# Optimization experiments

Measured on AMD Instinct MI355X. Metric: run time of the kernel, lower is better.

## Reference

```python
import jax, jax.numpy as jnp
import numpy as np

N_NODES = 50000
N_EDGES = 800000
IN_CH = 256
OUT_CH = 128
HID = 2 * OUT_CH  # 256
N_GRAPHS = 64


def setup_inputs() -> dict:
    key = jax.random.key(0)
    k = jax.random.split(key, 8)
    x = jax.random.normal(k[0], (N_NODES, IN_CH), dtype=jnp.float32)
    edge_index = jax.random.randint(k[1], (2, N_EDGES), 0, N_NODES, dtype=jnp.int64)
    batch = jnp.sort(jax.random.randint(k[2], (N_NODES,), 0, N_GRAPHS, dtype=jnp.int64))
    # GCNConv parameters (glorot-ish init)
    W1 = jax.random.normal(k[3], (IN_CH, HID), dtype=jnp.float32) / np.sqrt(IN_CH)
    b1 = jnp.zeros((HID,), dtype=jnp.float32)
    W2 = jax.random.normal(k[4], (HID, OUT_CH), dtype=jnp.float32) / np.sqrt(HID)
    b2 = jnp.zeros((OUT_CH,), dtype=jnp.float32)
    return {"x": x, "W1": W1, "b1": b1, "W2": W2, "b2": b2,
            "edge_index": edge_index, "batch": batch}


def _gcn_conv(x, W, b, src, dst, n):
    """PyG GCNConv: transform, then sym-normalized aggregation with self-loops."""
    h = x @ W  # [N, F_out]
    # degree over destination nodes, including the added self-loop
    deg = jnp.zeros((n,), dtype=h.dtype).at[dst].add(1.0) + 1.0
    dinv = jax.lax.rsqrt(deg)
    norm = dinv[src] * dinv[dst]            # [E]
    agg = jnp.zeros_like(h).at[dst].add(h[src] * norm[:, None])
    agg = agg + h * (1.0 / deg)[:, None]    # self-loop contribution: deg_i^{-1}
    return agg + b


def reference(x, W1, b1, W2, b2, edge_index, batch):
    src, dst = edge_index[0], edge_index[1]
    # dropout is identity in eval mode (training=False)
    h = jax.nn.elu(_gcn_conv(x, W1, b1, src, dst, N_NODES))
    h = _gcn_conv(h, W2, b2, src, dst, N_NODES)
    # global mean pool over graphs
    ones = jnp.ones((N_NODES,), dtype=h.dtype)
    counts = jax.ops.segment_sum(ones, batch, num_segments=N_GRAPHS)
    sums = jax.ops.segment_sum(h, batch, num_segments=N_GRAPHS)
    return sums / jnp.maximum(counts, 1.0)[:, None]
```

## Files before the change

### kernel.cpp

```cpp
#include <hip/hip_runtime.h>
#include <hip/hip_bf16.h>

#define N_NODES 50000
#define N_EDGES 800000
#define IN_CH 256
#define HID 256
#define OUT_CH 128
#define N_GRAPHS 64
#define SCAN_BLOCKS 196
#define M_PAD 50048
#define COUNT_BLOCKS 3125
#define CVTX_BLOCKS  12512
#define GEMM1_BLOCKS 782
#define SROW 50048
#define S_QUARTER 12512
#define GEMM2_BLOCKS 391
#define SBUILD_BLOCKS 256
#define T2_BLOCKS 391
#define T2_KC 128
#define RED_BLOCKS 128

typedef __bf16 bf16x8 __attribute__((ext_vector_type(8)));
typedef float f32x4 __attribute__((ext_vector_type(4)));
typedef float f32x2 __attribute__((ext_vector_type(2)));
typedef unsigned short u16x8 __attribute__((ext_vector_type(8)));

__device__ __forceinline__ float bf2f(unsigned short u) {
    union { unsigned int i; float f; } x; x.i = ((unsigned int)u) << 16; return x.f;
}
__device__ __forceinline__ unsigned short f2bf(float f) {
    union { float f; unsigned int i; } x; x.f = f;
    unsigned int r = x.i + 0x7FFFu + ((x.i >> 16) & 1u);
    return (unsigned short)(r >> 16);
}

__device__ __forceinline__ float lo_f(unsigned int u) {
    return __uint_as_float(u << 16);
}
__device__ __forceinline__ float hi_f(unsigned int u) {
    return __uint_as_float(u & 0xFFFF0000u);
}

__device__ __forceinline__ void load16(const void* g, void* l) {
    __builtin_amdgcn_global_load_lds(
        (const __attribute__((address_space(1))) void*)g,
        (__attribute__((address_space(3))) void*)l, 16, 0, 0);
}

__device__ __forceinline__ int rp(const int* __restrict__ rl,
                                  const int* __restrict__ boff, int i) {
    return rl[i] + boff[i >> 8];
}

__global__ __launch_bounds__(256) void count_cvtx_kernel(const int* __restrict__ ei,
                                                         int* __restrict__ cnt,
                                                         int* __restrict__ erank,
                                                         const float* __restrict__ x,
                                                         unsigned short* __restrict__ xb) {
    int b = blockIdx.x;
    if (b < COUNT_BLOCKS) {
        int e = b * 256 + threadIdx.x;
        erank[e] = atomicAdd(&cnt[ei[N_EDGES + e]], 1);
        return;
    }
    int i = (b - COUNT_BLOCKS) * 256 + threadIdx.x;
    ushort4 o;
    if (i < N_NODES * (IN_CH / 4)) {
        float4 v = ((const float4*)x)[i];
        o.x = f2bf(v.x); o.y = f2bf(v.y); o.z = f2bf(v.z); o.w = f2bf(v.w);
    } else {
        o = make_ushort4(0, 0, 0, 0);
    }
    ((ushort4*)xb)[i] = o;
}

__global__ __launch_bounds__(256) void scan_a_kernel(const int* __restrict__ cnt,
                                                     int* __restrict__ rl,
                                                     int* __restrict__ blocksum,
                                                     float* __restrict__ dinv,
                                                     float* __restrict__ invdeg,
                                                     const int* __restrict__ batch,
                                                     int* __restrict__ rstart) {
    __shared__ int tmp[256];
    int t = threadIdx.x;
    int i = blockIdx.x * 256 + t;
    int v = (i < N_NODES) ? cnt[i] : 0;
    int x = v;
    tmp[t] = x;
    __syncthreads();
    if (i < N_NODES) {
        int bg = batch[i];
        int bp = (i > 0) ? batch[i - 1] : -1;
        for (int g = bp + 1; g <= bg; g++) rstart[g] = i;
        if (i == N_NODES - 1)
            for (int g = bg + 1; g <= N_GRAPHS; g++) rstart[g] = N_NODES;
    }
#pragma unroll
    for (int off = 1; off < 256; off <<= 1) {
        int y = (t >= off) ? tmp[t - off] : 0;
        __syncthreads();
        x += y;
        tmp[t] = x;
        __syncthreads();
    }
    if (i <= N_NODES) rl[i] = x - v;
    if (i < N_NODES) {
        float d = (float)v + 1.0f;
        dinv[i] = rsqrtf(d);
        invdeg[i] = 1.0f / d;
    }
    if (t == 255) blocksum[blockIdx.x] = x;
}

__global__ __launch_bounds__(256) void scanb_cvtw_kernel(
        const int* __restrict__ blocksum, int* __restrict__ blockoff,
        const float* __restrict__ W1, const float* __restrict__ W2,
        unsigned short* __restrict__ w1t, unsigned short* __restrict__ w2t) {
    int t = threadIdx.x;
    if (blockIdx.x < 384) {
        int i = blockIdx.x * 256 + t;
        if (i < HID * IN_CH) {
            int n = i >> 8, k = i & 255;
            w1t[i] = f2bf(W1[k * HID + n]);
        } else {
            int j = i - HID * IN_CH;
            int n = j >> 8, k = j & 255;
            w2t[j] = f2bf(W2[k * OUT_CH + n]);
        }
        return;
    }
    __shared__ int tmp[256];
    int v = (t < SCAN_BLOCKS) ? blocksum[t] : 0;
    int x = v;
    tmp[t] = x;
    __syncthreads();
#pragma unroll
    for (int off = 1; off < 256; off <<= 1) {
        int y = (t >= off) ? tmp[t - off] : 0;
        __syncthreads();
        x += y;
        tmp[t] = x;
        __syncthreads();
    }
    if (t < SCAN_BLOCKS) blockoff[t] = x - v;
}

template <int TR>
__device__ __forceinline__ void gemm_body(const unsigned short* __restrict__ A,
                                          const unsigned short* __restrict__ Bt,
                                          unsigned short* __restrict__ C,
                                          int N, int bxx, int byy, char* As, char* Bs) {
    const int K = 256;
    int tid = threadIdx.x;
    int bm = bxx * 128;
    int bn = byy * 128;
    int lane = tid & 63, wave = tid >> 6;
    int lane15 = lane & 15, quad = lane >> 4;
    int wm0 = (wave >> 1) << 6;
    int wn0 = (wave & 1) << 6;

    int s1 = tid, s2 = tid + 256;
    int r1 = s1 >> 2, q1 = (s1 & 3) ^ ((r1 >> 1) & 3);
    int r2 = s2 >> 2, q2 = (s2 & 3) ^ ((r2 >> 1) & 3);
    const char* gA1 = (const char*)(A + (size_t)(bm + r1) * K) + (q1 << 4);
    const char* gA2 = (const char*)(A + (size_t)(bm + r2) * K) + (q2 << 4);
    const char* gB1 = (const char*)(Bt + (size_t)(bn + r1) * K) + (q1 << 4);
    const char* gB2 = (const char*)(Bt + (size_t)(bn + r2) * K) + (q2 << 4);
    char* lA1 = As + (wave << 10);
    char* lA2 = As + 4096 + (wave << 10);
    char* lB1 = Bs + (wave << 10);
    char* lB2 = Bs + 4096 + (wave << 10);

    int swm = (lane15 >> 1) & 3;
    f32x4 acc[4][4];
#pragma unroll
    for (int mt = 0; mt < 4; mt++)
#pragma unroll
        for (int nt = 0; nt < 4; nt++)
            acc[mt][nt] = (f32x4){0.f, 0.f, 0.f, 0.f};

    for (int k0 = 0; k0 < K; k0 += 32) {
        __syncthreads();
        load16(gA1 + (k0 << 1), lA1);
        load16(gA2 + (k0 << 1), lA2);
        load16(gB1 + (k0 << 1), lB1);
        load16(gB2 + (k0 << 1), lB2);
        __syncthreads();
        bf16x8 af[4], bfr[4];
#pragma unroll
        for (int t = 0; t < 4; t++) {
            int ra = wm0 + t * 16 + lane15;
            af[t] = *(const bf16x8*)(As + ra * 64 + ((quad ^ swm) << 4));
            int rb = wn0 + t * 16 + lane15;
            bfr[t] = *(const bf16x8*)(Bs + rb * 64 + ((quad ^ swm) << 4));
        }
#pragma unroll
        for (int mt = 0; mt < 4; mt++)
#pragma unroll
            for (int nt = 0; nt < 4; nt++)
                acc[mt][nt] = __builtin_amdgcn_mfma_f32_16x16x32_bf16(
                    af[mt], bfr[nt], acc[mt][nt], 0, 0, 0);
    }

#pragma unroll
    for (int mt = 0; mt < 4; mt++) {
        int rowb = bm + wm0 + mt * 16 + quad * 4;
#pragma unroll
        for (int nt = 0; nt < 4; nt++) {
            int col = bn + wn0 + nt * 16 + lane15;
            f32x4 a = acc[mt][nt];
            if (TR == 0) {
                C[(size_t)(rowb + 0) * N + col] = f2bf(a[0]);
                C[(size_t)(rowb + 1) * N + col] = f2bf(a[1]);
                C[(size_t)(rowb + 2) * N + col] = f2bf(a[2]);
                C[(size_t)(rowb + 3) * N + col] = f2bf(a[3]);
            } else {
                ushort4 o;
                o.x = f2bf(a[0]); o.y = f2bf(a[1]);
                o.z = f2bf(a[2]); o.w = f2bf(a[3]);
                *(ushort4*)(C + (size_t)col * M_PAD + rowb) = o;
            }
        }
    }
}

__global__ __launch_bounds__(256) void fill_gemm1_kernel(
        const int* __restrict__ ei,
        const int* __restrict__ rl,
        const int* __restrict__ boff,
        const int* __restrict__ erank,
        int2* __restrict__ edge2,
        const float* __restrict__ dinv,
        const unsigned short* __restrict__ xb,
        const unsigned short* __restrict__ w1t,
        unsigned short* __restrict__ h1b) {
    __shared__ char As[8192];
    __shared__ char Bs[8192];
    int b = blockIdx.x;
    if (b < GEMM1_BLOCKS) {
        gemm_body<0>(xb, w1t, h1b, HID, b % 391, b / 391, As, Bs);
        return;
    }
    int e = (b - GEMM1_BLOCKS) * 256 + threadIdx.x;
    if (e >= N_EDGES) return;
    int s = ei[e];
    int d = ei[N_EDGES + e];
    int p = rp(rl, boff, d) + erank[e];
    float w = dinv[s] * dinv[d];
    edge2[p] = make_int2(s, __float_as_int(w));
}

__global__ __launch_bounds__(256) void agg1_kernel(const unsigned short* __restrict__ h,
                                                   const float* __restrict__ bias,
                                                   const int* __restrict__ rl,
                                                   const int* __restrict__ boff,
                                                   const int2* __restrict__ edge2,
                                                   const float* __restrict__ invdeg,
                                                   unsigned short* __restrict__ out) {
    int node = blockIdx.x * 4 + (threadIdx.x >> 6);
    int lane = threadIdx.x & 63;
    if (node >= N_NODES) {
        if (node < M_PAD)
            ((ushort4*)out)[(size_t)node * 64 + lane] = make_ushort4(0, 0, 0, 0);
        return;
    }
    const uint2* h4 = (const uint2*)h;
    float id = invdeg[node];
    uint2 sv = h4[(size_t)node * 64 + lane];
    f32x4 acc = (f32x4){lo_f(sv.x) * id, hi_f(sv.x) * id,
                        lo_f(sv.y) * id, hi_f(sv.y) * id};
    int e0 = rp(rl, boff, node);
    int e1 = rp(rl, boff, node + 1);
    int e = e0;
    for (; e + 15 < e1; e += 16) {
        int2 ed[16];
        uint2 v[16];
#pragma unroll
        for (int j = 0; j < 16; j++) ed[j] = edge2[e + j];
#pragma unroll
        for (int j = 0; j < 16; j++) v[j] = h4[(size_t)ed[j].x * 64 + lane];
#pragma unroll
        for (int j = 0; j < 16; j++) {
            float w = __int_as_float(ed[j].y);
            f32x4 vf = (f32x4){lo_f(v[j].x), hi_f(v[j].x),
                               lo_f(v[j].y), hi_f(v[j].y)};
            acc += vf * w;
        }
    }
    for (; e + 7 < e1; e += 8) {
        int2 ed[8];
        uint2 v[8];
#pragma unroll
        for (int j = 0; j < 8; j++) ed[j] = edge2[e + j];
#pragma unroll
        for (int j = 0; j < 8; j++) v[j] = h4[(size_t)ed[j].x * 64 + lane];
#pragma unroll
        for (int j = 0; j < 8; j++) {
            float w = __int_as_float(ed[j].y);
            f32x4 vf = (f32x4){lo_f(v[j].x), hi_f(v[j].x),
                               lo_f(v[j].y), hi_f(v[j].y)};
            acc += vf * w;
        }
    }
    for (; e + 3 < e1; e += 4) {
        int2 ed[4];
        uint2 v[4];
#pragma unroll
        for (int j = 0; j < 4; j++) ed[j] = edge2[e + j];
#pragma unroll
        for (int j = 0; j < 4; j++) v[j] = h4[(size_t)ed[j].x * 64 + lane];
#pragma unroll
        for (int j = 0; j < 4; j++) {
            float w = __int_as_float(ed[j].y);
            f32x4 vf = (f32x4){lo_f(v[j].x), hi_f(v[j].x),
                               lo_f(v[j].y), hi_f(v[j].y)};
            acc += vf * w;
        }
    }
    for (; e < e1; e++) {
        int2 ed0 = edge2[e];
        float w0 = __int_as_float(ed0.y);
        uint2 v0 = h4[(size_t)ed0.x * 64 + lane];
        f32x4 vf = (f32x4){lo_f(v0.x), hi_f(v0.x), lo_f(v0.y), hi_f(v0.y)};
        acc += vf * w0;
    }
    float4 bb = ((const float4*)bias)[lane];
    acc[0] += bb.x; acc[1] += bb.y; acc[2] += bb.z; acc[3] += bb.w;
    acc[0] = acc[0] > 0.f ? acc[0] : expm1f(acc[0]);
    acc[1] = acc[1] > 0.f ? acc[1] : expm1f(acc[1]);
    acc[2] = acc[2] > 0.f ? acc[2] : expm1f(acc[2]);
    acc[3] = acc[3] > 0.f ? acc[3] : expm1f(acc[3]);
    ushort4 o;
    o.x = f2bf(acc[0]); o.y = f2bf(acc[1]); o.z = f2bf(acc[2]); o.w = f2bf(acc[3]);
    ((ushort4*)out)[(size_t)node * 64 + lane] = o;
}

__global__ __launch_bounds__(256) void gemm2_sbuild_kernel(
        const unsigned short* __restrict__ A,
        const unsigned short* __restrict__ Bt,
        unsigned short* __restrict__ C,
        const int2* __restrict__ edge2,
        const int* __restrict__ rl,
        const int* __restrict__ boff,
        const int* __restrict__ rstart,
        const float* __restrict__ invdeg,
        float* __restrict__ Sp) {
    __shared__ float srow[S_QUARTER];
    int b = blockIdx.x;
    if (b < GEMM2_BLOCKS) {
        gemm_body<1>(A, Bt, C, OUT_CH, b, 0, (char*)srow, (char*)srow + 8192);
        return;
    }
    int sb = b - GEMM2_BLOCKS;
    int g = sb >> 2;
    int base = (sb & 3) * S_QUARTER;
    int t = threadIdx.x;
    for (int i = t; i < S_QUARTER; i += 256) srow[i] = 0.f;
    int n0 = rstart[g], n1 = rstart[g + 1];
    __syncthreads();
    int e0 = rp(rl, boff, n0);
    int e1 = rp(rl, boff, n1);
    for (int e = e0 + t; e < e1; e += 256) {
        int2 ed = edge2[e];
        unsigned int s = (unsigned int)(ed.x - base);
        if (s < S_QUARTER)
            atomicAdd(&srow[s], __int_as_float(ed.y));
    }
    __syncthreads();
    float ic = 1.0f / fmaxf((float)(n1 - n0), 1.0f);
    float* Sg = Sp + (size_t)g * SROW + base;
    for (int i = t; i < S_QUARTER; i += 256) {
        float v = srow[i];
        int col = base + i;
        if (col >= n0 && col < n1) v += invdeg[col];
        Sg[i] = v * ic;
    }
}

__global__ __launch_bounds__(256) void t2_kernel(const float* __restrict__ Sp,
                                                 const unsigned short* __restrict__ h2t,
                                                 float* __restrict__ part) {
    int b = blockIdx.x;
    int k0 = b * T2_KC;
    int tid = threadIdx.x;
    int lane = tid & 63, wave = tid >> 6;
    int lane15 = lane & 15, quad = lane >> 4;
    int cb = wave << 5;
    f32x4 acc[4][2];
#pragma unroll
    for (int m = 0; m < 4; m++) {
        acc[m][0] = (f32x4){0.f, 0.f, 0.f, 0.f};
        acc[m][1] = (f32x4){0.f, 0.f, 0.f, 0.f};
    }
    const unsigned short* hr0 = h2t + (size_t)(cb + lane15) * M_PAD;
    const unsigned short* hr1 = h2t + (size_t)(cb + 16 + lane15) * M_PAD;
#pragma unroll
    for (int ks = 0; ks < T2_KC / 32; ks++) {
        int k = k0 + ks * 32 + quad * 8;
        bf16x8 b0 = *(const bf16x8*)(hr0 + k);
        bf16x8 b1 = *(const bf16x8*)(hr1 + k);
#pragma unroll
        for (int m = 0; m < 4; m++) {
            const float* ap = Sp + (size_t)(m * 16 + lane15) * SROW + k;
            f32x4 v0 = *(const f32x4*)ap;
            f32x4 v1 = *(const f32x4*)(ap + 4);
            u16x8 hu, lu;
#pragma unroll
            for (int j = 0; j < 4; j++) {
                unsigned int e0 = __float_as_uint(v0[j]);
                hu[j] = (unsigned short)(e0 >> 16);
                lu[j] = f2bf(v0[j] - __uint_as_float(e0 & 0xFFFF0000u));
                unsigned int e1 = __float_as_uint(v1[j]);
                hu[j + 4] = (unsigned short)(e1 >> 16);
                lu[j + 4] = f2bf(v1[j] - __uint_as_float(e1 & 0xFFFF0000u));
            }
            bf16x8 ah = __builtin_bit_cast(bf16x8, hu);
            bf16x8 al = __builtin_bit_cast(bf16x8, lu);
            acc[m][0] = __builtin_amdgcn_mfma_f32_16x16x32_bf16(ah, b0, acc[m][0], 0, 0, 0);
            acc[m][0] = __builtin_amdgcn_mfma_f32_16x16x32_bf16(al, b0, acc[m][0], 0, 0, 0);
            acc[m][1] = __builtin_amdgcn_mfma_f32_16x16x32_bf16(ah, b1, acc[m][1], 0, 0, 0);
            acc[m][1] = __builtin_amdgcn_mfma_f32_16x16x32_bf16(al, b1, acc[m][1], 0, 0, 0);
        }
    }
    float* pb = part + (size_t)b * (N_GRAPHS * OUT_CH);
#pragma unroll
    for (int m = 0; m < 4; m++) {
        int g0 = m * 16 + quad * 4;
#pragma unroll
        for (int nt = 0; nt < 2; nt++) {
            int c = cb + nt * 16 + lane15;
            f32x4 a = acc[m][nt];
#pragma unroll
            for (int j = 0; j < 4; j++)
                pb[(g0 + j) * OUT_CH + c] = a[j];
        }
    }
}

__global__ __launch_bounds__(256) void t2red_kernel(const float* __restrict__ part,
                                                    const float* __restrict__ b2,
                                                    const int* __restrict__ rstart,
                                                    float* __restrict__ out) {
    __shared__ float red[4][64];
    int tid = threadIdx.x;
    int q = tid >> 6, l = tid & 63;
    int o = blockIdx.x * 64 + l;
    float s = 0.f;
    for (int i = q; i < T2_BLOCKS; i += 4)
        s += part[(size_t)i * (N_GRAPHS * OUT_CH) + o];
    red[q][l] = s;
    __syncthreads();
    if (tid < 64) {
        float tot = red[0][l] + red[1][l] + red[2][l] + red[3][l];
        int g = o >> 7, c = o & 127;
        out[o] = (rstart[g + 1] > rstart[g]) ? tot + b2[c] : 0.f;
    }
}

extern "C" void kernel_launch(void* const* d_in, const int* in_sizes, int n_in,
                              void* d_out, int out_size, void* d_ws, size_t ws_size,
                              hipStream_t stream) {
    const float* x  = (const float*)d_in[0];
    const float* W1 = (const float*)d_in[1];
    const float* b1 = (const float*)d_in[2];
    const float* W2 = (const float*)d_in[3];
    const float* b2 = (const float*)d_in[4];
    const int*   ei = (const int*)d_in[5];
    const int*   batch = (const int*)d_in[6];
    float* out = (float*)d_out;

    unsigned short* xb  = (unsigned short*)d_ws;
    unsigned short* h1b = xb  + (size_t)M_PAD * IN_CH;
    unsigned short* hBb = h1b + (size_t)M_PAD * HID;
    unsigned short* h2t = hBb + (size_t)M_PAD * HID;
    unsigned short* w1t = h2t + (size_t)OUT_CH * M_PAD;
    unsigned short* w2t = w1t + HID * IN_CH;
    float* dinv   = (float*)(w2t + OUT_CH * HID);
    float* invdeg = dinv + N_NODES;
    int*   rl     = (int*)(invdeg + N_NODES);
    int2*  edge2  = (int2*)(rl + 50016);
    int*   cnt    = (int*)(edge2 + N_EDGES);
    int*   erank  = cnt + N_NODES;
    int*   blocksum = erank + N_EDGES;
    int*   blockoff = blocksum + 256;
    int*   rstart   = blockoff + 256;
    float* Sp     = (float*)(rstart + 80);
    float* part   = (float*)xb;

    hipMemsetAsync(cnt, 0, (size_t)N_NODES * 4, stream);

    count_cvtx_kernel<<<COUNT_BLOCKS + CVTX_BLOCKS, 256, 0, stream>>>(ei, cnt, erank, x, xb);
    scan_a_kernel<<<SCAN_BLOCKS, 256, 0, stream>>>(cnt, rl, blocksum, dinv, invdeg,
                                                   batch, rstart);
    scanb_cvtw_kernel<<<385, 256, 0, stream>>>(blocksum, blockoff, W1, W2, w1t, w2t);
    fill_gemm1_kernel<<<GEMM1_BLOCKS + COUNT_BLOCKS, 256, 0, stream>>>(
        ei, rl, blockoff, erank, edge2, dinv, xb, w1t, h1b);
    agg1_kernel<<<M_PAD / 4, 256, 0, stream>>>(h1b, b1, rl, blockoff,
                                               edge2, invdeg, hBb);
    gemm2_sbuild_kernel<<<GEMM2_BLOCKS + SBUILD_BLOCKS, 256, 0, stream>>>(
        hBb, w2t, h2t, edge2, rl, blockoff, rstart, invdeg, Sp);
    t2_kernel<<<T2_BLOCKS, 256, 0, stream>>>(Sp, h2t, part);
    t2red_kernel<<<RED_BLOCKS, 256, 0, stream>>>(part, b2, rstart, out);
}
```

Before: 297.3 us.

## Restructure layer-1 aggregation to thread-per-node over 32-channel column slices

The layer-1 gather/aggregate kernel changes from one wavefront per node (each lane reading 4 channels) to one thread per node per 32-channel slice. Eight slice groups each handle all nodes, and every thread processes two nodes spaced half the node range apart. Each neighbor row is now fetched as four 16-byte loads per thread, and edge metadata is read per thread rather than broadcast across a wave. The goal is wider per-thread memory accesses and more independent work per thread. The cost is uncoalesced access patterns across a wave, divergence from differing node degrees, and a shallower unroll (2 edges) for hiding gather latency.

Measured after the change: 427.2 us. 43.7% more time.

```diff
diff --git a/kernel.cpp b/kernel.cpp
--- a/kernel.cpp
+++ b/kernel.cpp
@@ -19,6 +19,9 @@
 #define T2_BLOCKS 391
 #define T2_KC 128
 #define RED_BLOCKS 128
+#define AGG_HALF 25024
+#define AGG_CHUNKS 98
+#define AGG_BLOCKS (8 * AGG_CHUNKS)
 
 typedef __bf16 bf16x8 __attribute__((ext_vector_type(8)));
 typedef float f32x4 __attribute__((ext_vector_type(4)));
@@ -250,6 +253,12 @@
     edge2[p] = make_int2(s, __float_as_int(w));
 }
 
+#define EXP2(Q, I, W) \
+    acc[I]     += (f32x2){lo_f(Q.x), hi_f(Q.x)} * W; \
+    acc[I + 1] += (f32x2){lo_f(Q.y), hi_f(Q.y)} * W; \
+    acc[I + 2] += (f32x2){lo_f(Q.z), hi_f(Q.z)} * W; \
+    acc[I + 3] += (f32x2){lo_f(Q.w), hi_f(Q.w)} * W;
+
 __global__ __launch_bounds__(256) void agg1_kernel(const unsigned short* __restrict__ h,
                                                    const float* __restrict__ bias,
                                                    const int* __restrict__ rl,
@@ -257,82 +266,59 @@
                                                    const int2* __restrict__ edge2,
                                                    const float* __restrict__ invdeg,
                                                    unsigned short* __restrict__ out) {
-    int node = blockIdx.x * 4 + (threadIdx.x >> 6);
-    int lane = threadIdx.x & 63;
-    if (node >= N_NODES) {
-        if (node < M_PAD)
-            ((ushort4*)out)[(size_t)node * 64 + lane] = make_ushort4(0, 0, 0, 0);
-        return;
-    }
-    const uint2* h4 = (const uint2*)h;
-    float id = invdeg[node];
-    uint2 sv = h4[(size_t)node * 64 + lane];
-    f32x4 acc = (f32x4){lo_f(sv.x) * id, hi_f(sv.x) * id,
-                        lo_f(sv.y) * id, hi_f(sv.y) * id};
-    int e0 = rp(rl, boff, node);
-    int e1 = rp(rl, boff, node + 1);
-    int e = e0;
-    for (; e + 15 < e1; e += 16) {
-        int2 ed[16];
-        uint2 v[16];
-#pragma unroll
-        for (int j = 0; j < 16; j++) ed[j] = edge2[e + j];
-#pragma unroll
-        for (int j = 0; j < 16; j++) v[j] = h4[(size_t)ed[j].x * 64 + lane];
-#pragma unroll
-        for (int j = 0; j < 16; j++) {
-            float w = __int_as_float(ed[j].y);
-            f32x4 vf = (f32x4){lo_f(v[j].x), hi_f(v[j].x),
-                               lo_f(v[j].y), hi_f(v[j].y)};
-            acc += vf * w;
-        }
-    }
-    for (; e + 7 < e1; e += 8) {
-        int2 ed[8];
-        uint2 v[8];
-#pragma unroll
-        for (int j = 0; j < 8; j++) ed[j] = edge2[e + j];
-#pragma unroll
-        for (int j = 0; j < 8; j++) v[j] = h4[(size_t)ed[j].x * 64 + lane];
-#pragma unroll
-        for (int j = 0; j < 8; j++) {
-            float w = __int_as_float(ed[j].y);
-            f32x4 vf = (f32x4){lo_f(v[j].x), hi_f(v[j].x),
-                               lo_f(v[j].y), hi_f(v[j].y)};
-            acc += vf * w;
-        }
-    }
-    for (; e + 3 < e1; e += 4) {
-        int2 ed[4];
-        uint2 v[4];
-#pragma unroll
-        for (int j = 0; j < 4; j++) ed[j] = edge2[e + j];
-#pragma unroll
-        for (int j = 0; j < 4; j++) v[j] = h4[(size_t)ed[j].x * 64 + lane];
-#pragma unroll
-        for (int j = 0; j < 4; j++) {
-            float w = __int_as_float(ed[j].y);
-            f32x4 vf = (f32x4){lo_f(v[j].x), hi_f(v[j].x),
-                               lo_f(v[j].y), hi_f(v[j].y)};
-            acc += vf * w;
-        }
-    }
-    for (; e < e1; e++) {
-        int2 ed0 = edge2[e];
-        float w0 = __int_as_float(ed0.y);
-        uint2 v0 = h4[(size_t)ed0.x * 64 + lane];
-        f32x4 vf = (f32x4){lo_f(v0.x), hi_f(v0.x), lo_f(v0.y), hi_f(v0.y)};
-        acc += vf * w0;
-    }
-    float4 bb = ((const float4*)bias)[lane];
-    acc[0] += bb.x; acc[1] += bb.y; acc[2] += bb.z; acc[3] += bb.w;
-    acc[0] = acc[0] > 0.f ? acc[0] : expm1f(acc[0]);
-    acc[1] = acc[1] > 0.f ? acc[1] : expm1f(acc[1]);
-    acc[2] = acc[2] > 0.f ? acc[2] : expm1f(acc[2]);
-    acc[3] = acc[3] > 0.f ? acc[3] : expm1f(acc[3]);
-    ushort4 o;
-    o.x = f2bf(acc[0]); o.y = f2bf(acc[1]); o.z = f2bf(acc[2]); o.w = f2bf(acc[3]);
-    ((ushort4*)out)[(size_t)node * 64 + lane] = o;
+    int cs = (blockIdx.x & 7) * 32;
+    int na = (blockIdx.x >> 3) * 256 + threadIdx.x;
+    if (na >= AGG_HALF) return;
+    for (int hh = 0; hh < 2; hh++) {
+        int node = na + hh * AGG_HALF;
+        uint4* op = (uint4*)(out + (size_t)node * 256 + cs);
+        if (node >= N_NODES) {
+            uint4 z = make_uint4(0, 0, 0, 0);
+            op[0] = z; op[1] = z; op[2] = z; op[3] = z;
+            continue;
+        }
+        f32x2 acc[16];
+        const uint4* sp = (const uint4*)(h + (size_t)node * 256 + cs);
+        uint4 s0 = sp[0], s1 = sp[1], s2 = sp[2], s3 = sp[3];
+        float id = invdeg[node];
+#pragma unroll
+        for (int i = 0; i < 16; i++) acc[i] = (f32x2){0.f, 0.f};
+        EXP2(s0, 0, id); EXP2(s1, 4, id); EXP2(s2, 8, id); EXP2(s3, 12, id);
+        int e0 = rp(rl, boff, node);
+        int e1 = rp(rl, boff, node + 1);
+        int e = e0;
+        for (; e + 1 < e1; e += 2) {
+            int2 edA = edge2[e], edB = edge2[e + 1];
+            const uint4* pA = (const uint4*)(h + (size_t)edA.x * 256 + cs);
+            const uint4* pB = (const uint4*)(h + (size_t)edB.x * 256 + cs);
+            uint4 a0 = pA[0], a1 = pA[1], a2 = pA[2], a3 = pA[3];
+            uint4 b0 = pB[0], b1 = pB[1], b2 = pB[2], b3 = pB[3];
+            float wA = __int_as_float(edA.y);
+            float wB = __int_as_float(edB.y);
+            EXP2(a0, 0, wA); EXP2(a1, 4, wA); EXP2(a2, 8, wA); EXP2(a3, 12, wA);
+            EXP2(b0, 0, wB); EXP2(b1, 4, wB); EXP2(b2, 8, wB); EXP2(b3, 12, wB);
+        }
+        if (e < e1) {
+            int2 ed = edge2[e];
+            const uint4* p = (const uint4*)(h + (size_t)ed.x * 256 + cs);
+            uint4 a0 = p[0], a1 = p[1], a2 = p[2], a3 = p[3];
+            float w = __int_as_float(ed.y);
+            EXP2(a0, 0, w); EXP2(a1, 4, w); EXP2(a2, 8, w); EXP2(a3, 12, w);
+        }
+        const f32x2* bp = (const f32x2*)(bias + cs);
+        unsigned int ou[16];
+#pragma unroll
+        for (int i = 0; i < 16; i++) {
+            f32x2 a = acc[i] + bp[i];
+            a[0] = a[0] > 0.f ? a[0] : expm1f(a[0]);
+            a[1] = a[1] > 0.f ? a[1] : expm1f(a[1]);
+            ou[i] = (unsigned int)f2bf(a[0]) | ((unsigned int)f2bf(a[1]) << 16);
+        }
+        op[0] = make_uint4(ou[0], ou[1], ou[2], ou[3]);
+        op[1] = make_uint4(ou[4], ou[5], ou[6], ou[7]);
+        op[2] = make_uint4(ou[8], ou[9], ou[10], ou[11]);
+        op[3] = make_uint4(ou[12], ou[13], ou[14], ou[15]);
+    }
 }
 
 __global__ __launch_bounds__(256) void gemm2_sbuild_kernel(
@@ -495,8 +481,8 @@
     scanb_cvtw_kernel<<<385, 256, 0, stream>>>(blocksum, blockoff, W1, W2, w1t, w2t);
     fill_gemm1_kernel<<<GEMM1_BLOCKS + COUNT_BLOCKS, 256, 0, stream>>>(
         ei, rl, blockoff, erank, edge2, dinv, xb, w1t, h1b);
-    agg1_kernel<<<M_PAD / 4, 256, 0, stream>>>(h1b, b1, rl, blockoff,
-                                               edge2, invdeg, hBb);
+    agg1_kernel<<<AGG_BLOCKS, 256, 0, stream>>>(h1b, b1, rl, blockoff,
+                                                edge2, invdeg, hBb);
     gemm2_sbuild_kernel<<<GEMM2_BLOCKS + SBUILD_BLOCKS, 256, 0, stream>>>(
         hBb, w2t, h2t, edge2, rl, blockoff, rstart, invdeg, Sp);
     t2_kernel<<<T2_BLOCKS, 256, 0, stream>>>(Sp, h2t, part);
```

## Store GEMM1 output in 32-column slices and aggregate one slice per block

Applied to the files above, without the earlier changes.

GEMM1 now writes h1 in a sliced layout, with 32-column chunks stored contiguously per node. The layer-1 aggregation kernel assigns each block to one column slice and 64 nodes, with 16 threads per node, so the gathered rows for one slice form a smaller working set that fits better in cache. Edge records are read with nontemporal loads so they do not displace those rows. The cost is that each node's edge list is re-read eight times (once per slice), and each lane does narrower 4-byte gathers.

Result: slower. 330.4 us (+11.2%).

```diff
diff --git a/kernel.cpp b/kernel.cpp
--- a/kernel.cpp
+++ b/kernel.cpp
@@ -19,6 +19,7 @@
 #define T2_BLOCKS 391
 #define T2_KC 128
 #define RED_BLOCKS 128
+#define AGG1_BLOCKS 6256
 
 typedef __bf16 bf16x8 __attribute__((ext_vector_type(8)));
 typedef float f32x4 __attribute__((ext_vector_type(4)));
@@ -39,6 +40,14 @@
 }
 __device__ __forceinline__ float hi_f(unsigned int u) {
     return __uint_as_float(u & 0xFFFF0000u);
+}
+
+__device__ __forceinline__ int2 nt_edge(const int2* p) {
+    long long v = __builtin_nontemporal_load((const long long*)p);
+    int2 r;
+    r.x = (int)(v & 0xFFFFFFFFll);
+    r.y = (int)(v >> 32);
+    return r;
 }
 
 __device__ __forceinline__ void load16(const void* g, void* l) {
@@ -214,11 +223,18 @@
                 C[(size_t)(rowb + 1) * N + col] = f2bf(a[1]);
                 C[(size_t)(rowb + 2) * N + col] = f2bf(a[2]);
                 C[(size_t)(rowb + 3) * N + col] = f2bf(a[3]);
-            } else {
+            } else if (TR == 1) {
                 ushort4 o;
                 o.x = f2bf(a[0]); o.y = f2bf(a[1]);
                 o.z = f2bf(a[2]); o.w = f2bf(a[3]);
                 *(ushort4*)(C + (size_t)col * M_PAD + rowb) = o;
+            } else {
+                unsigned short* base =
+                    C + ((size_t)(col >> 5) * M_PAD + rowb) * 32 + (col & 31);
+                base[0]  = f2bf(a[0]);
+                base[32] = f2bf(a[1]);
+                base[64] = f2bf(a[2]);
+                base[96] = f2bf(a[3]);
             }
         }
     }
@@ -238,7 +254,7 @@
     __shared__ char Bs[8192];
     int b = blockIdx.x;
     if (b < GEMM1_BLOCKS) {
-        gemm_body<0>(xb, w1t, h1b, HID, b % 391, b / 391, As, Bs);
+        gemm_body<2>(xb, w1t, h1b, HID, b % 391, b / 391, As, Bs);
         return;
     }
     int e = (b - GEMM1_BLOCKS) * 256 + threadIdx.x;
@@ -257,82 +273,62 @@
                                                    const int2* __restrict__ edge2,
                                                    const float* __restrict__ invdeg,
                                                    unsigned short* __restrict__ out) {
-    int node = blockIdx.x * 4 + (threadIdx.x >> 6);
-    int lane = threadIdx.x & 63;
-    if (node >= N_NODES) {
-        if (node < M_PAD)
-            ((ushort4*)out)[(size_t)node * 64 + lane] = make_ushort4(0, 0, 0, 0);
-        return;
-    }
-    const uint2* h4 = (const uint2*)h;
-    float id = invdeg[node];
-    uint2 sv = h4[(size_t)node * 64 + lane];
-    f32x4 acc = (f32x4){lo_f(sv.x) * id, hi_f(sv.x) * id,
-                        lo_f(sv.y) * id, hi_f(sv.y) * id};
-    int e0 = rp(rl, boff, node);
-    int e1 = rp(rl, boff, node + 1);
-    int e = e0;
-    for (; e + 15 < e1; e += 16) {
-        int2 ed[16];
-        uint2 v[16];
-#pragma unroll
-        for (int j = 0; j < 16; j++) ed[j] = edge2[e + j];
-#pragma unroll
-        for (int j = 0; j < 16; j++) v[j] = h4[(size_t)ed[j].x * 64 + lane];
-#pragma unroll
-        for (int j = 0; j < 16; j++) {
-            float w = __int_as_float(ed[j].y);
-            f32x4 vf = (f32x4){lo_f(v[j].x), hi_f(v[j].x),
-                               lo_f(v[j].y), hi_f(v[j].y)};
-            acc += vf * w;
-        }
-    }
-    for (; e + 7 < e1; e += 8) {
-        int2 ed[8];
-        uint2 v[8];
-#pragma unroll
-        for (int j = 0; j < 8; j++) ed[j] = edge2[e + j];
-#pragma unroll
-        for (int j = 0; j < 8; j++) v[j] = h4[(size_t)ed[j].x * 64 + lane];
-#pragma unroll
-        for (int j = 0; j < 8; j++) {
-            float w = __int_as_float(ed[j].y);
-            f32x4 vf = (f32x4){lo_f(v[j].x), hi_f(v[j].x),
-                               lo_f(v[j].y), hi_f(v[j].y)};
-            acc += vf * w;
-        }
-    }
-    for (; e + 3 < e1; e += 4) {
-        int2 ed[4];
-        uint2 v[4];
-#pragma unroll
-        for (int j = 0; j < 4; j++) ed[j] = edge2[e + j];
-#pragma unroll
-        for (int j = 0; j < 4; j++) v[j] = h4[(size_t)ed[j].x * 64 + lane];
-#pragma unroll
-        for (int j = 0; j < 4; j++) {
-            float w = __int_as_float(ed[j].y);
-            f32x4 vf = (f32x4){lo_f(v[j].x), hi_f(v[j].x),
-                               lo_f(v[j].y), hi_f(v[j].y)};
-            acc += vf * w;
-        }
-    }
-    for (; e < e1; e++) {
-        int2 ed0 = edge2[e];
-        float w0 = __int_as_float(ed0.y);
-        uint2 v0 = h4[(size_t)ed0.x * 64 + lane];
-        f32x4 vf = (f32x4){lo_f(v0.x), hi_f(v0.x), lo_f(v0.y), hi_f(v0.y)};
-        acc += vf * w0;
-    }
-    float4 bb = ((const float4*)bias)[lane];
-    acc[0] += bb.x; acc[1] += bb.y; acc[2] += bb.z; acc[3] += bb.w;
-    acc[0] = acc[0] > 0.f ? acc[0] : expm1f(acc[0]);
-    acc[1] = acc[1] > 0.f ? acc[1] : expm1f(acc[1]);
-    acc[2] = acc[2] > 0.f ? acc[2] : expm1f(acc[2]);
-    acc[3] = acc[3] > 0.f ? acc[3] : expm1f(acc[3]);
-    ushort4 o;
-    o.x = f2bf(acc[0]); o.y = f2bf(acc[1]); o.z = f2bf(acc[2]); o.w = f2bf(acc[3]);
-    ((ushort4*)out)[(size_t)node * 64 + lane] = o;
+    int slice = blockIdx.x & 7;
+    int cs = slice * 32;
+    const unsigned int* hs = (const unsigned int*)(h + (size_t)slice * M_PAD * 32);
+    int grp = threadIdx.x >> 4;
+    int lph = threadIdx.x & 15;
+    int nb = (blockIdx.x >> 3) * 64;
+    float2 bb = ((const float2*)(bias + cs))[lph];
+#pragma unroll
+    for (int it = 0; it < 4; it++) {
+        int node = nb + it * 16 + grp;
+        unsigned int* op = (unsigned int*)(out + (size_t)node * 256 + cs) + lph;
+        if (node >= N_NODES) { *op = 0u; continue; }
+        unsigned int svu = hs[node * 16 + lph];
+        float id = invdeg[node];
+        f32x2 acc = (f32x2){lo_f(svu) * id, hi_f(svu) * id};
+        int e0 = rp(rl, boff, node);
+        int e1 = rp(rl, boff, node + 1);
+        int e = e0;
+        for (; e + 7 < e1; e += 8) {
+            int2 ed[8];
+            unsigned int v[8];
+#pragma unroll
+            for (int j = 0; j < 8; j++) ed[j] = nt_edge(edge2 + e + j);
+#pragma unroll
+            for (int j = 0; j < 8; j++) v[j] = hs[(size_t)ed[j].x * 16 + lph];
+#pragma unroll
+            for (int j = 0; j < 8; j++) {
+                float w = __int_as_float(ed[j].y);
+                acc += (f32x2){lo_f(v[j]), hi_f(v[j])} * w;
+            }
+        }
+        for (; e + 3 < e1; e += 4) {
+            int2 ed[4];
+            unsigned int v[4];
+#pragma unroll
+            for (int j = 0; j < 4; j++) ed[j] = nt_edge(edge2 + e + j);
+#pragma unroll
+            for (int j = 0; j < 4; j++) v[j] = hs[(size_t)ed[j].x * 16 + lph];
+#pragma unroll
+            for (int j = 0; j < 4; j++) {
+                float w = __int_as_float(ed[j].y);
+                acc += (f32x2){lo_f(v[j]), hi_f(v[j])} * w;
+            }
+        }
+        for (; e < e1; e++) {
+            int2 ed = nt_edge(edge2 + e);
+            unsigned int v = hs[(size_t)ed.x * 16 + lph];
+            float w = __int_as_float(ed.y);
+            acc += (f32x2){lo_f(v), hi_f(v)} * w;
+        }
+        float a0 = acc[0] + bb.x;
+        float a1 = acc[1] + bb.y;
+        a0 = a0 > 0.f ? a0 : expm1f(a0);
+        a1 = a1 > 0.f ? a1 : expm1f(a1);
+        *op = (unsigned int)f2bf(a0) | ((unsigned int)f2bf(a1) << 16);
+    }
 }
 
 __global__ __launch_bounds__(256) void gemm2_sbuild_kernel(
@@ -495,8 +491,8 @@
     scanb_cvtw_kernel<<<385, 256, 0, stream>>>(blocksum, blockoff, W1, W2, w1t, w2t);
     fill_gemm1_kernel<<<GEMM1_BLOCKS + COUNT_BLOCKS, 256, 0, stream>>>(
         ei, rl, blockoff, erank, edge2, dinv, xb, w1t, h1b);
-    agg1_kernel<<<M_PAD / 4, 256, 0, stream>>>(h1b, b1, rl, blockoff,
-                                               edge2, invdeg, hBb);
+    agg1_kernel<<<AGG1_BLOCKS, 256, 0, stream>>>(h1b, b1, rl, blockoff,
+                                                 edge2, invdeg, hBb);
     gemm2_sbuild_kernel<<<GEMM2_BLOCKS + SBUILD_BLOCKS, 256, 0, stream>>>(
         hBb, w2t, h2t, edge2, rl, blockoff, rstart, invdeg, Sp);
     t2_kernel<<<T2_BLOCKS, 256, 0, stream>>>(Sp, h2t, part);
```

## Move S-matrix build into agg1 launch and weight conversion into count launch

Applied to the files above, without the earlier changes.

The pooled-aggregation matrix build is moved out of the gemm2 launch and into the agg1 launch, split into eighths instead of quarters so each block uses a smaller shared buffer (512 blocks). The W1/W2 bf16 transpose moves from the scanb kernel into the first count/convert kernel, leaving scanb as a single-block scan. The aim is to rebalance work across launches so the atomic-heavy S build overlaps the gather-bound agg1 rather than the GEMM, and the weight conversion is off the short scan step. The risk is that the S-build blocks are scheduled first and delay agg1. Gemm2 now runs without them and can achieve higher occupancy.

Result: no change. 301.1 us (+1.3%).

```diff
diff --git a/kernel.cpp b/kernel.cpp
--- a/kernel.cpp
+++ b/kernel.cpp
@@ -11,11 +11,12 @@
 #define M_PAD 50048
 #define COUNT_BLOCKS 3125
 #define CVTX_BLOCKS  12512
+#define CVTW_BLOCKS  384
 #define GEMM1_BLOCKS 782
 #define SROW 50048
-#define S_QUARTER 12512
+#define S_EIGHTH 6256
+#define SBUILD8_BLOCKS 512
 #define GEMM2_BLOCKS 391
-#define SBUILD_BLOCKS 256
 #define T2_BLOCKS 391
 #define T2_KC 128
 #define RED_BLOCKS 128
@@ -52,26 +53,39 @@
     return rl[i] + boff[i >> 8];
 }
 
-__global__ __launch_bounds__(256) void count_cvtx_kernel(const int* __restrict__ ei,
-                                                         int* __restrict__ cnt,
-                                                         int* __restrict__ erank,
-                                                         const float* __restrict__ x,
-                                                         unsigned short* __restrict__ xb) {
+__global__ __launch_bounds__(256) void count_cvtx_cvtw_kernel(
+        const int* __restrict__ ei, int* __restrict__ cnt, int* __restrict__ erank,
+        const float* __restrict__ x, unsigned short* __restrict__ xb,
+        const float* __restrict__ W1, const float* __restrict__ W2,
+        unsigned short* __restrict__ w1t, unsigned short* __restrict__ w2t) {
     int b = blockIdx.x;
     if (b < COUNT_BLOCKS) {
         int e = b * 256 + threadIdx.x;
         erank[e] = atomicAdd(&cnt[ei[N_EDGES + e]], 1);
         return;
     }
-    int i = (b - COUNT_BLOCKS) * 256 + threadIdx.x;
-    ushort4 o;
-    if (i < N_NODES * (IN_CH / 4)) {
-        float4 v = ((const float4*)x)[i];
-        o.x = f2bf(v.x); o.y = f2bf(v.y); o.z = f2bf(v.z); o.w = f2bf(v.w);
+    b -= COUNT_BLOCKS;
+    if (b < CVTX_BLOCKS) {
+        int i = b * 256 + threadIdx.x;
+        ushort4 o;
+        if (i < N_NODES * (IN_CH / 4)) {
+            float4 v = ((const float4*)x)[i];
+            o.x = f2bf(v.x); o.y = f2bf(v.y); o.z = f2bf(v.z); o.w = f2bf(v.w);
+        } else {
+            o = make_ushort4(0, 0, 0, 0);
+        }
+        ((ushort4*)xb)[i] = o;
+        return;
+    }
+    int i = (b - CVTX_BLOCKS) * 256 + threadIdx.x;
+    if (i < HID * IN_CH) {
+        int n = i >> 8, k = i & 255;
+        w1t[i] = f2bf(W1[k * HID + n]);
     } else {
-        o = make_ushort4(0, 0, 0, 0);
-    }
-    ((ushort4*)xb)[i] = o;
+        int j = i - HID * IN_CH;
+        int n = j >> 8, k = j & 255;
+        w2t[j] = f2bf(W2[k * OUT_CH + n]);
+    }
 }
 
 __global__ __launch_bounds__(256) void scan_a_kernel(const int* __restrict__ cnt,
@@ -112,24 +126,10 @@
     if (t == 255) blocksum[blockIdx.x] = x;
 }
 
-__global__ __launch_bounds__(256) void scanb_cvtw_kernel(
-        const int* __restrict__ blocksum, int* __restrict__ blockoff,
-        const float* __restrict__ W1, const float* __restrict__ W2,
-        unsigned short* __restrict__ w1t, unsigned short* __restrict__ w2t) {
+__global__ __launch_bounds__(256) void scanb1_kernel(const int* __restrict__ blocksum,
+                                                     int* __restrict__ blockoff) {
+    __shared__ int tmp[256];
     int t = threadIdx.x;
-    if (blockIdx.x < 384) {
-        int i = blockIdx.x * 256 + t;
-        if (i < HID * IN_CH) {
-            int n = i >> 8, k = i & 255;
-            w1t[i] = f2bf(W1[k * HID + n]);
-        } else {
-            int j = i - HID * IN_CH;
-            int n = j >> 8, k = j & 255;
-            w2t[j] = f2bf(W2[k * OUT_CH + n]);
-        }
-        return;
-    }
-    __shared__ int tmp[256];
     int v = (t < SCAN_BLOCKS) ? blocksum[t] : 0;
     int x = v;
     tmp[t] = x;
@@ -250,14 +250,45 @@
     edge2[p] = make_int2(s, __float_as_int(w));
 }
 
-__global__ __launch_bounds__(256) void agg1_kernel(const unsigned short* __restrict__ h,
-                                                   const float* __restrict__ bias,
-                                                   const int* __restrict__ rl,
-                                                   const int* __restrict__ boff,
-                                                   const int2* __restrict__ edge2,
-                                                   const float* __restrict__ invdeg,
-                                                   unsigned short* __restrict__ out) {
-    int node = blockIdx.x * 4 + (threadIdx.x >> 6);
+__global__ __launch_bounds__(256) void agg1_sbuild_kernel(
+        const unsigned short* __restrict__ h,
+        const float* __restrict__ bias,
+        const int* __restrict__ rl,
+        const int* __restrict__ boff,
+        const int2* __restrict__ edge2,
+        const float* __restrict__ invdeg,
+        unsigned short* __restrict__ out,
+        const int* __restrict__ rstart,
+        float* __restrict__ Sp) {
+    __shared__ float srow[S_EIGHTH];
+    int b = blockIdx.x;
+    if (b < SBUILD8_BLOCKS) {
+        int g = b >> 3;
+        int base = (b & 7) * S_EIGHTH;
+        int t = threadIdx.x;
+        for (int i = t; i < S_EIGHTH; i += 256) srow[i] = 0.f;
+        int n0 = rstart[g], n1 = rstart[g + 1];
+        __syncthreads();
+        int e0 = rp(rl, boff, n0);
+        int e1 = rp(rl, boff, n1);
+        for (int e = e0 + t; e < e1; e += 256) {
+            int2 ed = edge2[e];
+            unsigned int s = (unsigned int)(ed.x - base);
+            if (s < S_EIGHTH)
+                atomicAdd(&srow[s], __int_as_float(ed.y));
+        }
+        __syncthreads();
+        float ic = 1.0f / fmaxf((float)(n1 - n0), 1.0f);
+        float* Sg = Sp + (size_t)g * SROW + base;
+        for (int i = t; i < S_EIGHTH; i += 256) {
+            float v = srow[i];
+            int col = base + i;
+            if (col >= n0 && col < n1) v += invdeg[col];
+            Sg[i] = v * ic;
+        }
+        return;
+    }
+    int node = (b - SBUILD8_BLOCKS) * 4 + (threadIdx.x >> 6);
     int lane = threadIdx.x & 63;
     if (node >= N_NODES) {
         if (node < M_PAD)
@@ -335,46 +366,13 @@
     ((ushort4*)out)[(size_t)node * 64 + lane] = o;
 }
 
-__global__ __launch_bounds__(256) void gemm2_sbuild_kernel(
+__global__ __launch_bounds__(256) void gemm2_kernel(
         const unsigned short* __restrict__ A,
         const unsigned short* __restrict__ Bt,
-        unsigned short* __restrict__ C,
-        const int2* __restrict__ edge2,
-        const int* __restrict__ rl,
-        const int* __restrict__ boff,
-        const int* __restrict__ rstart,
-        const float* __restrict__ invdeg,
-        float* __restrict__ Sp) {
-    __shared__ float srow[S_QUARTER];
-    int b = blockIdx.x;
-    if (b < GEMM2_BLOCKS) {
-        gemm_body<1>(A, Bt, C, OUT_CH, b, 0, (char*)srow, (char*)srow + 8192);
-        return;
-    }
-    int sb = b - GEMM2_BLOCKS;
-    int g = sb >> 2;
-    int base = (sb & 3) * S_QUARTER;
-    int t = threadIdx.x;
-    for (int i = t; i < S_QUARTER; i += 256) srow[i] = 0.f;
-    int n0 = rstart[g], n1 = rstart[g + 1];
-    __syncthreads();
-    int e0 = rp(rl, boff, n0);
-    int e1 = rp(rl, boff, n1);
-    for (int e = e0 + t; e < e1; e += 256) {
-        int2 ed = edge2[e];
-        unsigned int s = (unsigned int)(ed.x - base);
-        if (s < S_QUARTER)
-            atomicAdd(&srow[s], __int_as_float(ed.y));
-    }
-    __syncthreads();
-    float ic = 1.0f / fmaxf((float)(n1 - n0), 1.0f);
-    float* Sg = Sp + (size_t)g * SROW + base;
-    for (int i = t; i < S_QUARTER; i += 256) {
-        float v = srow[i];
-        int col = base + i;
-        if (col >= n0 && col < n1) v += invdeg[col];
-        Sg[i] = v * ic;
-    }
+        unsigned short* __restrict__ C) {
+    __shared__ char As[8192];
+    __shared__ char Bs[8192];
+    gemm_body<1>(A, Bt, C, OUT_CH, blockIdx.x, 0, As, Bs);
 }
 
 __global__ __launch_bounds__(256) void t2_kernel(const float* __restrict__ Sp,
@@ -489,16 +487,16 @@
 
     hipMemsetAsync(cnt, 0, (size_t)N_NODES * 4, stream);
 
-    count_cvtx_kernel<<<COUNT_BLOCKS + CVTX_BLOCKS, 256, 0, stream>>>(ei, cnt, erank, x, xb);
+    count_cvtx_cvtw_kernel<<<COUNT_BLOCKS + CVTX_BLOCKS + CVTW_BLOCKS, 256, 0, stream>>>(
+        ei, cnt, erank, x, xb, W1, W2, w1t, w2t);
     scan_a_kernel<<<SCAN_BLOCKS, 256, 0, stream>>>(cnt, rl, blocksum, dinv, invdeg,
                                                    batch, rstart);
-    scanb_cvtw_kernel<<<385, 256, 0, stream>>>(blocksum, blockoff, W1, W2, w1t, w2t);
+    scanb1_kernel<<<1, 256, 0, stream>>>(blocksum, blockoff);
     fill_gemm1_kernel<<<GEMM1_BLOCKS + COUNT_BLOCKS, 256, 0, stream>>>(
         ei, rl, blockoff, erank, edge2, dinv, xb, w1t, h1b);
-    agg1_kernel<<<M_PAD / 4, 256, 0, stream>>>(h1b, b1, rl, blockoff,
-                                               edge2, invdeg, hBb);
-    gemm2_sbuild_kernel<<<GEMM2_BLOCKS + SBUILD_BLOCKS, 256, 0, stream>>>(
-        hBb, w2t, h2t, edge2, rl, blockoff, rstart, invdeg, Sp);
+    agg1_sbuild_kernel<<<SBUILD8_BLOCKS + M_PAD / 4, 256, 0, stream>>>(
+        h1b, b1, rl, blockoff, edge2, invdeg, hBb, rstart, Sp);
+    gemm2_kernel<<<GEMM2_BLOCKS, 256, 0, stream>>>(hBb, w2t, h2t);
     t2_kernel<<<T2_BLOCKS, 256, 0, stream>>>(Sp, h2t, part);
     t2red_kernel<<<RED_BLOCKS, 256, 0, stream>>>(part, b2, rstart, out);
 }
```
